# Kernel optimization log

Hardware: AMD Instinct MI355X
Metric: run time of the kernel (lower is better)

The kernel has to match this reference:

```python
import jax, jax.numpy as jnp
import numpy as np

D_MODEL = 384
HEAD_SIZE = 64
B, T = 64, 512


def setup_inputs() -> dict:
    key = jax.random.key(0)
    kx, kq, kk, kv = jax.random.split(key, 4)
    x = jax.random.normal(kx, (B, T, D_MODEL), dtype=jnp.float32)
    Wq = jax.random.normal(kq, (D_MODEL, HEAD_SIZE), dtype=jnp.float32) * 0.02
    Wk = jax.random.normal(kk, (D_MODEL, HEAD_SIZE), dtype=jnp.float32) * 0.02
    Wv = jax.random.normal(kv, (D_MODEL, HEAD_SIZE), dtype=jnp.float32) * 0.02
    return {"x": x, "Wq": Wq, "Wk": Wk, "Wv": Wv}


def reference(x, Wq, Wk, Wv):
    # x: [B, T, C]; projections (bias-free linear layers)
    q = jnp.einsum("btc,ch->bth", x, Wq)  # [B, T, H]
    k = jnp.einsum("btc,ch->bth", x, Wk)
    v = jnp.einsum("btc,ch->bth", x, Wv)
    Tn = x.shape[1]
    scale = 1.0 / jnp.sqrt(jnp.float32(k.shape[-1]))
    wei = jnp.einsum("bqh,bkh->bqk", q, k) * scale  # [B, T, T]
    causal = jnp.tril(jnp.ones((Tn, Tn), dtype=bool))
    wei = jnp.where(causal, wei, -jnp.inf)
    wei = jax.nn.softmax(wei, axis=-1)
    # dropout omitted (eval mode) for deterministic reference
    out = jnp.einsum("bqk,bkh->bqh", wei, v)  # [B, T, H]
    return out
```

## Files before the change

kernel.cpp:

```cpp
#include <hip/hip_runtime.h>
#include <math.h>

#define NB 64
#define NT 512
#define NC 384
#define NH 64

typedef __attribute__((ext_vector_type(8))) short bf16x8;
typedef __attribute__((ext_vector_type(4))) float f32x4;

__device__ __forceinline__ unsigned short f2bf(float f) {
  unsigned int u = __float_as_uint(f);
  return (unsigned short)((u + 0x7FFFu + ((u >> 16) & 1u)) >> 16);
}
__device__ __forceinline__ unsigned int pk2bf(float a, float b) {
  return (unsigned int)f2bf(a) | ((unsigned int)f2bf(b) << 16);
}

__global__ __launch_bounds__(256) void wtrans_kernel(
    const float* __restrict__ Wq, const float* __restrict__ Wk,
    const float* __restrict__ Wv, unsigned short* __restrict__ Wt) {
  int id = blockIdx.x * 256 + threadIdx.x;
  if (id >= 3 * NC * NH) return;
  int m = id / (NC * NH);
  int r = id % (NC * NH);
  int c = r / NH;
  int h = r % NH;
  const float* W = (m == 0) ? Wq : ((m == 1) ? Wk : Wv);
  Wt[(m * NH + h) * NC + c] = f2bf(W[c * NH + h]);
}

#define XS 392
__global__ __launch_bounds__(384, 3) void proj_kernel(
    const float* __restrict__ x, const unsigned short* __restrict__ Wt,
    unsigned short* __restrict__ q, unsigned short* __restrict__ k,
    unsigned short* __restrict__ vt) {
  __shared__ unsigned short xs[64 * XS];
  const int t = threadIdx.x;
  const int m0 = blockIdx.x * 64;
  const int w = t / 64, l = t & 63, mi = l & 15, quad = l >> 4;

#pragma unroll 4
  for (int i = 0; i < 16; ++i) {
    int u = t + i * 384;
    int row = u / 96;
    int cp = (u % 96) * 4;
    float4 a = *(const float4*)(x + (size_t)(m0 + row) * NC + cp);
    ushort4 bb;
    bb.x = f2bf(a.x); bb.y = f2bf(a.y); bb.z = f2bf(a.z); bb.w = f2bf(a.w);
    *(ushort4*)&xs[row * XS + cp] = bb;
  }

  bf16x8 bfr[2][12];
#pragma unroll
  for (int ntl = 0; ntl < 2; ++ntl) {
    const unsigned short* wr =
        Wt + (size_t)((w * 2 + ntl) * 16 + mi) * NC + quad * 8;
#pragma unroll
    for (int kc = 0; kc < 12; ++kc)
      bfr[ntl][kc] = *(const bf16x8*)(wr + kc * 32);
  }
  __syncthreads();

  f32x4 acc[2][4];
  const f32x4 zero = {0.f, 0.f, 0.f, 0.f};
#pragma unroll
  for (int i = 0; i < 2; ++i)
#pragma unroll
    for (int j = 0; j < 4; ++j) acc[i][j] = zero;

#pragma unroll
  for (int msub = 0; msub < 4; ++msub) {
#pragma unroll
    for (int kc = 0; kc < 12; ++kc) {
      bf16x8 a = *(const bf16x8*)&xs[(msub * 16 + mi) * XS + kc * 32 + quad * 8];
      acc[0][msub] =
          __builtin_amdgcn_mfma_f32_16x16x32_bf16(a, bfr[0][kc], acc[0][msub], 0, 0, 0);
      acc[1][msub] =
          __builtin_amdgcn_mfma_f32_16x16x32_bf16(a, bfr[1][kc], acc[1][msub], 0, 0, 0);
    }
  }

  if (w < 4) {
    unsigned short* dst = (w < 2) ? q : k;
    const float sc = (w < 2) ? 0.125f : 1.0f;
#pragma unroll
    for (int ntl = 0; ntl < 2; ++ntl) {
      int tile = w * 2 + ntl;
      int h = (tile & 3) * 16 + mi;
#pragma unroll
      for (int msub = 0; msub < 4; ++msub)
#pragma unroll
        for (int r = 0; r < 4; ++r)
          dst[(size_t)(m0 + msub * 16 + quad * 4 + r) * NH + h] =
              f2bf(acc[ntl][msub][r] * sc);
    }
  } else {
    int bb = m0 >> 9, t0 = m0 & 511;
#pragma unroll
    for (int ntl = 0; ntl < 2; ++ntl) {
      int tile = w * 2 + ntl;
      int h = (tile & 3) * 16 + mi;
#pragma unroll
      for (int msub = 0; msub < 4; ++msub) {
        ushort4 s;
        s.x = f2bf(acc[ntl][msub][0]);
        s.y = f2bf(acc[ntl][msub][1]);
        s.z = f2bf(acc[ntl][msub][2]);
        s.w = f2bf(acc[ntl][msub][3]);
        *(ushort4*)&vt[((size_t)bb * NH + h) * NT + t0 + msub * 16 + quad * 4] = s;
      }
    }
  }
}

#define PSTR 72
__global__ __launch_bounds__(64) void attn_kernel(
    const unsigned short* __restrict__ q, const unsigned short* __restrict__ k,
    const unsigned short* __restrict__ vt, float* __restrict__ out) {
  __shared__ unsigned short ps[16 * PSTR];
  const int l = threadIdx.x;
  const int mi = l & 15, quad = l >> 4;
  const int bx = blockIdx.x;
  const int qi = 31 - (bx >> 6);
  const int b = bx & 63;

  const unsigned short* qrow = q + ((size_t)b * NT + qi * 16 + mi) * NH;
  bf16x8 qb0 = *(const bf16x8*)(qrow + quad * 8);
  bf16x8 qb1 = *(const bf16x8*)(qrow + 32 + quad * 8);

  f32x4 accO[4];
  const f32x4 zero = {0.f, 0.f, 0.f, 0.f};
#pragma unroll
  for (int i = 0; i < 4; ++i) accO[i] = zero;
  float mrow = -INFINITY, lrow = 0.f;

  const int ktmax = (qi * 16 + 15) >> 6;
  for (int kt = 0; kt <= ktmax; ++kt) {
    const unsigned short* kb = k + ((size_t)b * NT + kt * 64) * NH;
    const unsigned short* vb = vt + (size_t)b * NH * NT + kt * 64;
    bf16x8 ka0[4], ka1[4], va0[4], va1[4];
#pragma unroll
    for (int nt = 0; nt < 4; ++nt) {
      const unsigned short* kr = kb + (size_t)(nt * 16 + mi) * NH + quad * 8;
      ka0[nt] = *(const bf16x8*)kr;
      ka1[nt] = *(const bf16x8*)(kr + 32);
      const unsigned short* vr = vb + (size_t)(nt * 16 + mi) * NT + quad * 8;
      va0[nt] = *(const bf16x8*)vr;
      va1[nt] = *(const bf16x8*)(vr + 32);
    }

    float p[4][4];
#pragma unroll
    for (int nt = 0; nt < 4; ++nt) {
      f32x4 z = zero;
      z = __builtin_amdgcn_mfma_f32_16x16x32_bf16(ka0[nt], qb0, z, 0, 0, 0);
      z = __builtin_amdgcn_mfma_f32_16x16x32_bf16(ka1[nt], qb1, z, 0, 0, 0);
#pragma unroll
      for (int r = 0; r < 4; ++r) p[nt][r] = z[r];
    }

    if (kt == ktmax) {
#pragma unroll
      for (int nt = 0; nt < 4; ++nt)
#pragma unroll
        for (int r = 0; r < 4; ++r)
          if (kt * 64 + nt * 16 + quad * 4 + r > qi * 16 + mi)
            p[nt][r] = -INFINITY;
    }

    float vmax = -INFINITY;
#pragma unroll
    for (int nt = 0; nt < 4; ++nt)
#pragma unroll
      for (int r = 0; r < 4; ++r) vmax = fmaxf(vmax, p[nt][r]);
    vmax = fmaxf(vmax, __shfl_xor(vmax, 16));
    vmax = fmaxf(vmax, __shfl_xor(vmax, 32));
    float mn = fmaxf(mrow, vmax);
    float alpha = __expf(mrow - mn);
    mrow = mn;

    float rsum = 0.f;
#pragma unroll
    for (int nt = 0; nt < 4; ++nt)
#pragma unroll
      for (int r = 0; r < 4; ++r) {
        p[nt][r] = __expf(p[nt][r] - mn);
        rsum += p[nt][r];
      }
    rsum += __shfl_xor(rsum, 16);
    rsum += __shfl_xor(rsum, 32);
    lrow = lrow * alpha + rsum;

#pragma unroll
    for (int nt = 0; nt < 4; ++nt) {
      uint2 pk;
      pk.x = pk2bf(p[nt][0], p[nt][1]);
      pk.y = pk2bf(p[nt][2], p[nt][3]);
      *(uint2*)&ps[mi * PSTR + nt * 16 + quad * 4] = pk;
    }
    bf16x8 pa0 = *(const bf16x8*)&ps[mi * PSTR + quad * 8];
    bf16x8 pa1 = *(const bf16x8*)&ps[mi * PSTR + 32 + quad * 8];

    float av[4];
#pragma unroll
    for (int r = 0; r < 4; ++r) av[r] = __shfl(alpha, quad * 4 + r);
#pragma unroll
    for (int hi = 0; hi < 4; ++hi)
#pragma unroll
      for (int r = 0; r < 4; ++r) accO[hi][r] *= av[r];

#pragma unroll
    for (int hi = 0; hi < 4; ++hi) {
      accO[hi] = __builtin_amdgcn_mfma_f32_16x16x32_bf16(pa0, va0[hi], accO[hi], 0, 0, 0);
      accO[hi] = __builtin_amdgcn_mfma_f32_16x16x32_bf16(pa1, va1[hi], accO[hi], 0, 0, 0);
    }
  }

  float inv = 1.f / lrow;
  const size_t obase = ((size_t)b * NT + qi * 16) * NH;
#pragma unroll
  for (int r = 0; r < 4; ++r) {
    float iv = __shfl(inv, quad * 4 + r);
#pragma unroll
    for (int hi = 0; hi < 4; ++hi)
      out[obase + (size_t)(quad * 4 + r) * NH + hi * 16 + mi] = accO[hi][r] * iv;
  }
}

extern "C" void kernel_launch(void* const* d_in, const int* in_sizes, int n_in,
                              void* d_out, int out_size, void* d_ws, size_t ws_size,
                              hipStream_t stream) {
  const float* x  = (const float*)d_in[0];
  const float* Wq = (const float*)d_in[1];
  const float* Wk = (const float*)d_in[2];
  const float* Wv = (const float*)d_in[3];

  unsigned short* Wt = (unsigned short*)d_ws;
  unsigned short* qb = Wt + 192 * 384;
  unsigned short* kb = qb + 32768 * 64;
  unsigned short* vtb = kb + 32768 * 64;
  float* out = (float*)d_out;

  wtrans_kernel<<<288, 256, 0, stream>>>(Wq, Wk, Wv, Wt);
  proj_kernel<<<512, 384, 0, stream>>>(x, Wt, qb, kb, vtb);
  attn_kernel<<<2048, 64, 0, stream>>>(qb, kb, vtb, out);
}
```

Baseline: 121.4 us.

## Double-buffer K/V register loads in attention and use hardware bf16 pack conversion

The attention loop now prefetches the next 64-key K/V tile into a second register set while computing on the current one, so global load latency is hidden behind MFMA and softmax work. The per-row rescale factors are broadcast through a small shared array instead of four shuffles. Software round-to-nearest bf16 conversion is replaced by the v_cvt_pk_bf16_f32 instruction in both kernels. The double buffer roughly doubles K/V register use, and the launch bound of 2 may cause spills or lower occupancy.

Result: no change. 122.9 us (+1.3%).

```diff
diff --git a/kernel.cpp b/kernel.cpp
--- a/kernel.cpp
+++ b/kernel.cpp
@@ -13,8 +13,10 @@
   unsigned int u = __float_as_uint(f);
   return (unsigned short)((u + 0x7FFFu + ((u >> 16) & 1u)) >> 16);
 }
-__device__ __forceinline__ unsigned int pk2bf(float a, float b) {
-  return (unsigned int)f2bf(a) | ((unsigned int)f2bf(b) << 16);
+__device__ __forceinline__ unsigned int cvt_pk_bf16(float lo, float hi) {
+  unsigned int r;
+  asm("v_cvt_pk_bf16_f32 %0, %1, %2" : "=v"(r) : "v"(lo), "v"(hi));
+  return r;
 }
 
 __global__ __launch_bounds__(256) void wtrans_kernel(
@@ -46,9 +48,10 @@
     int row = u / 96;
     int cp = (u % 96) * 4;
     float4 a = *(const float4*)(x + (size_t)(m0 + row) * NC + cp);
-    ushort4 bb;
-    bb.x = f2bf(a.x); bb.y = f2bf(a.y); bb.z = f2bf(a.z); bb.w = f2bf(a.w);
-    *(ushort4*)&xs[row * XS + cp] = bb;
+    uint2 bbu;
+    bbu.x = cvt_pk_bf16(a.x, a.y);
+    bbu.y = cvt_pk_bf16(a.z, a.w);
+    *(uint2*)&xs[row * XS + cp] = bbu;
   }
 
   bf16x8 bfr[2][12];
@@ -89,11 +92,17 @@
       int tile = w * 2 + ntl;
       int h = (tile & 3) * 16 + mi;
 #pragma unroll
-      for (int msub = 0; msub < 4; ++msub)
-#pragma unroll
-        for (int r = 0; r < 4; ++r)
-          dst[(size_t)(m0 + msub * 16 + quad * 4 + r) * NH + h] =
-              f2bf(acc[ntl][msub][r] * sc);
+      for (int msub = 0; msub < 4; ++msub) {
+        unsigned int u01 =
+            cvt_pk_bf16(acc[ntl][msub][0] * sc, acc[ntl][msub][1] * sc);
+        unsigned int u23 =
+            cvt_pk_bf16(acc[ntl][msub][2] * sc, acc[ntl][msub][3] * sc);
+        size_t base = (size_t)(m0 + msub * 16 + quad * 4) * NH + h;
+        dst[base] = (unsigned short)u01;
+        dst[base + NH] = (unsigned short)(u01 >> 16);
+        dst[base + 2 * NH] = (unsigned short)u23;
+        dst[base + 3 * NH] = (unsigned short)(u23 >> 16);
+      }
     }
   } else {
     int bb = m0 >> 9, t0 = m0 & 511;
@@ -103,22 +112,21 @@
       int h = (tile & 3) * 16 + mi;
 #pragma unroll
       for (int msub = 0; msub < 4; ++msub) {
-        ushort4 s;
-        s.x = f2bf(acc[ntl][msub][0]);
-        s.y = f2bf(acc[ntl][msub][1]);
-        s.z = f2bf(acc[ntl][msub][2]);
-        s.w = f2bf(acc[ntl][msub][3]);
-        *(ushort4*)&vt[((size_t)bb * NH + h) * NT + t0 + msub * 16 + quad * 4] = s;
+        uint2 s_;
+        s_.x = cvt_pk_bf16(acc[ntl][msub][0], acc[ntl][msub][1]);
+        s_.y = cvt_pk_bf16(acc[ntl][msub][2], acc[ntl][msub][3]);
+        *(uint2*)&vt[((size_t)bb * NH + h) * NT + t0 + msub * 16 + quad * 4] = s_;
       }
     }
   }
 }
 
 #define PSTR 72
-__global__ __launch_bounds__(64) void attn_kernel(
+__global__ __launch_bounds__(64, 2) void attn_kernel(
     const unsigned short* __restrict__ q, const unsigned short* __restrict__ k,
     const unsigned short* __restrict__ vt, float* __restrict__ out) {
   __shared__ unsigned short ps[16 * PSTR];
+  __shared__ __align__(16) float alpha_s[16];
   const int l = threadIdx.x;
   const int mi = l & 15, quad = l >> 4;
   const int bx = blockIdx.x;
@@ -135,97 +143,116 @@
   for (int i = 0; i < 4; ++i) accO[i] = zero;
   float mrow = -INFINITY, lrow = 0.f;
 
+  const unsigned short* kbase = k + (size_t)b * NT * NH;
+  const unsigned short* vbase = vt + (size_t)b * NH * NT;
   const int ktmax = (qi * 16 + 15) >> 6;
-  for (int kt = 0; kt <= ktmax; ++kt) {
-    const unsigned short* kb = k + ((size_t)b * NT + kt * 64) * NH;
-    const unsigned short* vb = vt + (size_t)b * NH * NT + kt * 64;
-    bf16x8 ka0[4], ka1[4], va0[4], va1[4];
-#pragma unroll
-    for (int nt = 0; nt < 4; ++nt) {
-      const unsigned short* kr = kb + (size_t)(nt * 16 + mi) * NH + quad * 8;
-      ka0[nt] = *(const bf16x8*)kr;
-      ka1[nt] = *(const bf16x8*)(kr + 32);
-      const unsigned short* vr = vb + (size_t)(nt * 16 + mi) * NT + quad * 8;
-      va0[nt] = *(const bf16x8*)vr;
-      va1[nt] = *(const bf16x8*)(vr + 32);
-    }
-
-    float p[4][4];
-#pragma unroll
-    for (int nt = 0; nt < 4; ++nt) {
-      f32x4 z = zero;
-      z = __builtin_amdgcn_mfma_f32_16x16x32_bf16(ka0[nt], qb0, z, 0, 0, 0);
-      z = __builtin_amdgcn_mfma_f32_16x16x32_bf16(ka1[nt], qb1, z, 0, 0, 0);
-#pragma unroll
-      for (int r = 0; r < 4; ++r) p[nt][r] = z[r];
-    }
-
-    if (kt == ktmax) {
-#pragma unroll
-      for (int nt = 0; nt < 4; ++nt)
-#pragma unroll
-        for (int r = 0; r < 4; ++r)
-          if (kt * 64 + nt * 16 + quad * 4 + r > qi * 16 + mi)
-            p[nt][r] = -INFINITY;
-    }
-
-    float vmax = -INFINITY;
-#pragma unroll
-    for (int nt = 0; nt < 4; ++nt)
-#pragma unroll
-      for (int r = 0; r < 4; ++r) vmax = fmaxf(vmax, p[nt][r]);
-    vmax = fmaxf(vmax, __shfl_xor(vmax, 16));
-    vmax = fmaxf(vmax, __shfl_xor(vmax, 32));
-    float mn = fmaxf(mrow, vmax);
-    float alpha = __expf(mrow - mn);
-    mrow = mn;
-
-    float rsum = 0.f;
-#pragma unroll
-    for (int nt = 0; nt < 4; ++nt)
-#pragma unroll
-      for (int r = 0; r < 4; ++r) {
-        p[nt][r] = __expf(p[nt][r] - mn);
-        rsum += p[nt][r];
-      }
-    rsum += __shfl_xor(rsum, 16);
-    rsum += __shfl_xor(rsum, 32);
-    lrow = lrow * alpha + rsum;
-
-#pragma unroll
-    for (int nt = 0; nt < 4; ++nt) {
-      uint2 pk;
-      pk.x = pk2bf(p[nt][0], p[nt][1]);
-      pk.y = pk2bf(p[nt][2], p[nt][3]);
-      *(uint2*)&ps[mi * PSTR + nt * 16 + quad * 4] = pk;
-    }
-    bf16x8 pa0 = *(const bf16x8*)&ps[mi * PSTR + quad * 8];
-    bf16x8 pa1 = *(const bf16x8*)&ps[mi * PSTR + 32 + quad * 8];
-
-    float av[4];
-#pragma unroll
-    for (int r = 0; r < 4; ++r) av[r] = __shfl(alpha, quad * 4 + r);
+
+  bf16x8 ka0A[4], ka1A[4], va0A[4], va1A[4];
+  bf16x8 ka0B[4], ka1B[4], va0B[4], va1B[4];
+
+#define LOADKV(KA0, KA1, VA0, VA1, KT)                                        \
+  {                                                                           \
+    const unsigned short* kb_ = kbase + (size_t)(KT) * 64 * NH;               \
+    const unsigned short* vb_ = vbase + (KT) * 64;                            \
+    _Pragma("unroll") for (int nt_ = 0; nt_ < 4; ++nt_) {                     \
+      const unsigned short* kr_ =                                             \
+          kb_ + (size_t)(nt_ * 16 + mi) * NH + quad * 8;                      \
+      KA0[nt_] = *(const bf16x8*)kr_;                                         \
+      KA1[nt_] = *(const bf16x8*)(kr_ + 32);                                  \
+      const unsigned short* vr_ =                                             \
+          vb_ + (size_t)(nt_ * 16 + mi) * NT + quad * 8;                      \
+      VA0[nt_] = *(const bf16x8*)vr_;                                         \
+      VA1[nt_] = *(const bf16x8*)(vr_ + 32);                                  \
+    }                                                                         \
+  }
+
+#define COMPUTE(KA0, KA1, VA0, VA1, KT)                                       \
+  {                                                                           \
+                         \
+    float p_[4][4];                                                           \
+    _Pragma("unroll") for (int nt_ = 0; nt_ < 4; ++nt_) {                     \
+      f32x4 z_ = zero;                                                        \
+      z_ = __builtin_amdgcn_mfma_f32_16x16x32_bf16(KA0[nt_], qb0, z_, 0, 0, 0); \
+      z_ = __builtin_amdgcn_mfma_f32_16x16x32_bf16(KA1[nt_], qb1, z_, 0, 0, 0); \
+      _Pragma("unroll") for (int r_ = 0; r_ < 4; ++r_) p_[nt_][r_] = z_[r_];  \
+    }                                                                         \
+    if ((KT) == ktmax) {                    \
+      _Pragma("unroll") for (int nt_ = 0; nt_ < 4; ++nt_)                     \
+          _Pragma("unroll") for (int r_ = 0; r_ < 4; ++r_)                    \
+              if ((KT)*64 + nt_ * 16 + quad * 4 + r_ > qi * 16 + mi)          \
+        p_[nt_][r_] = -INFINITY;                                              \
+    }                                                                         \
+    float vmax_ = -INFINITY;                                                  \
+    _Pragma("unroll") for (int nt_ = 0; nt_ < 4; ++nt_)                       \
+        _Pragma("unroll") for (int r_ = 0; r_ < 4; ++r_)                      \
+            vmax_ = fmaxf(vmax_, p_[nt_][r_]);                                \
+    vmax_ = fmaxf(vmax_, __shfl_xor(vmax_, 16));                              \
+    vmax_ = fmaxf(vmax_, __shfl_xor(vmax_, 32));                              \
+    float mn_ = fmaxf(mrow, vmax_);                                           \
+    float alpha_ = __expf(mrow - mn_);                                        \
+    mrow = mn_;                                                               \
+    float rsum_ = 0.f;                                                        \
+    _Pragma("unroll") for (int nt_ = 0; nt_ < 4; ++nt_)                       \
+        _Pragma("unroll") for (int r_ = 0; r_ < 4; ++r_) {                    \
+      p_[nt_][r_] = __expf(p_[nt_][r_] - mn_);                                \
+      rsum_ += p_[nt_][r_];                                                   \
+    }                                                                         \
+    rsum_ += __shfl_xor(rsum_, 16);                                           \
+    rsum_ += __shfl_xor(rsum_, 32);                                           \
+    lrow = lrow * alpha_ + rsum_;                                             \
+                     \
+    if (quad == 0) alpha_s[mi] = alpha_;                                      \
+    _Pragma("unroll") for (int nt_ = 0; nt_ < 4; ++nt_) {                     \
+      uint2 pk_;                                                              \
+      pk_.x = cvt_pk_bf16(p_[nt_][0], p_[nt_][1]);                            \
+      pk_.y = cvt_pk_bf16(p_[nt_][2], p_[nt_][3]);                            \
+      *(uint2*)&ps[mi * PSTR + nt_ * 16 + quad * 4] = pk_;                    \
+    }                                                                         \
+    bf16x8 pa0_ = *(const bf16x8*)&ps[mi * PSTR + quad * 8];                  \
+    bf16x8 pa1_ = *(const bf16x8*)&ps[mi * PSTR + 32 + quad * 8];             \
+    f32x4 av_ = *(const f32x4*)&alpha_s[quad * 4];                            \
+    _Pragma("unroll") for (int hi_ = 0; hi_ < 4; ++hi_)                       \
+        _Pragma("unroll") for (int r_ = 0; r_ < 4; ++r_)                      \
+            accO[hi_][r_] *= av_[r_];                                         \
+                    \
+    _Pragma("unroll") for (int hi_ = 0; hi_ < 4; ++hi_) {                     \
+      accO[hi_] = __builtin_amdgcn_mfma_f32_16x16x32_bf16(pa0_, VA0[hi_],     \
+                                                          accO[hi_], 0, 0, 0); \
+      accO[hi_] = __builtin_amdgcn_mfma_f32_16x16x32_bf16(pa1_, VA1[hi_],     \
+                                                          accO[hi_], 0, 0, 0); \
+    }                                                                         \
+  }
+
+  LOADKV(ka0A, ka1A, va0A, va1A, 0);
+  int kt = 0;
+  while (kt < ktmax) {
+    LOADKV(ka0B, ka1B, va0B, va1B, kt + 1);
+    COMPUTE(ka0A, ka1A, va0A, va1A, kt);
+    ++kt;
+    if (kt < ktmax) {
+      LOADKV(ka0A, ka1A, va0A, va1A, kt + 1);
+      COMPUTE(ka0B, ka1B, va0B, va1B, kt);
+      ++kt;
+    } else {
+      COMPUTE(ka0B, ka1B, va0B, va1B, kt);
+      ++kt;
+    }
+  }
+  if (kt == ktmax) COMPUTE(ka0A, ka1A, va0A, va1A, kt);
+
+  float inv = 1.f / lrow;
+  if (quad == 0) alpha_s[mi] = inv;
+  f32x4 iv4 = *(const f32x4*)&alpha_s[quad * 4];
+  const size_t obase = ((size_t)b * NT + qi * 16) * NH;
+#pragma unroll
+  for (int r = 0; r < 4; ++r) {
 #pragma unroll
     for (int hi = 0; hi < 4; ++hi)
-#pragma unroll
-      for (int r = 0; r < 4; ++r) accO[hi][r] *= av[r];
-
-#pragma unroll
-    for (int hi = 0; hi < 4; ++hi) {
-      accO[hi] = __builtin_amdgcn_mfma_f32_16x16x32_bf16(pa0, va0[hi], accO[hi], 0, 0, 0);
-      accO[hi] = __builtin_amdgcn_mfma_f32_16x16x32_bf16(pa1, va1[hi], accO[hi], 0, 0, 0);
-    }
-  }
-
-  float inv = 1.f / lrow;
-  const size_t obase = ((size_t)b * NT + qi * 16) * NH;
-#pragma unroll
-  for (int r = 0; r < 4; ++r) {
-    float iv = __shfl(inv, quad * 4 + r);
-#pragma unroll
-    for (int hi = 0; hi < 4; ++hi)
-      out[obase + (size_t)(quad * 4 + r) * NH + hi * 16 + mi] = accO[hi][r] * iv;
-  }
+      out[obase + (size_t)(quad * 4 + r) * NH + hi * 16 + mi] =
+          accO[hi][r] * iv4[r];
+  }
+#undef LOADKV
+#undef COMPUTE
 }
 
 extern "C" void kernel_launch(void* const* d_in, const int* in_sizes, int n_in,
```
